# Performance work log

Hardware: AMD Instinct MI355X
Metric: run time of the kernel (lower is better)

Reference implementation:

```python
import jax, jax.numpy as jnp
import numpy as np

N = 100000      # nodes
E = 1600000     # edges (before self-loops)
IN = 128        # in_channels
HID = 64        # hidden_channels
HEADS = 2
G = 64          # graphs in batch
NEG_SLOPE = 0.2


def setup_inputs() -> dict:
    key = jax.random.key(0)
    ks = jax.random.split(key, 13)
    x = jax.random.normal(ks[0], (N, IN), dtype=jnp.float32)
    edge_index = jax.random.randint(ks[1], (2, E), 0, N, dtype=jnp.int64)
    batch = jnp.sort(jax.random.randint(ks[2], (N,), 0, G, dtype=jnp.int64))
    # GATConv 1: in=128 -> 64 per head, heads=2, concat
    W1 = jax.random.normal(ks[3], (IN, HEADS * HID), dtype=jnp.float32) / np.sqrt(IN)
    a1_src = jax.random.normal(ks[4], (HEADS, HID), dtype=jnp.float32) / np.sqrt(HID)
    a1_dst = jax.random.normal(ks[5], (HEADS, HID), dtype=jnp.float32) / np.sqrt(HID)
    b1 = jnp.zeros((HEADS * HID,), dtype=jnp.float32)
    # GATConv 2: in=128 -> 64, heads=1, mean (concat=False)
    W2 = jax.random.normal(ks[6], (HEADS * HID, 1 * HID), dtype=jnp.float32) / np.sqrt(HEADS * HID)
    a2_src = jax.random.normal(ks[7], (1, HID), dtype=jnp.float32) / np.sqrt(HID)
    a2_dst = jax.random.normal(ks[8], (1, HID), dtype=jnp.float32) / np.sqrt(HID)
    b2 = jnp.zeros((HID,), dtype=jnp.float32)
    # final Linear(64, 1)
    Wlin = jax.random.normal(ks[9], (HID, 1), dtype=jnp.float32) / np.sqrt(HID)
    blin = jnp.zeros((1,), dtype=jnp.float32)
    return {"x": x, "edge_index": edge_index, "batch": batch,
            "W1": W1, "a1_src": a1_src, "a1_dst": a1_dst, "b1": b1,
            "W2": W2, "a2_src": a2_src, "a2_dst": a2_dst, "b2": b2,
            "Wlin": Wlin, "blin": blin}


def gat_conv(x, src, dst, W, a_src, a_dst, bias, heads, out_dim, concat):
    # x: [N, F_in]; src/dst: [E'] (self-loops already included, PyG default)
    h = (x @ W).reshape(-1, heads, out_dim)                 # [N, H, C]
    alpha_s = jnp.sum(h * a_src[None], axis=-1)             # [N, H]
    alpha_d = jnp.sum(h * a_dst[None], axis=-1)             # [N, H]
    e = alpha_s[src] + alpha_d[dst]                         # [E', H]
    e = jnp.where(e > 0, e, NEG_SLOPE * e)                  # LeakyReLU(0.2)
    # segment softmax over incoming edges of each destination node
    e_max = jax.ops.segment_max(e, dst, num_segments=N)     # [N, H]
    e_exp = jnp.exp(e - e_max[dst])
    denom = jax.ops.segment_sum(e_exp, dst, num_segments=N) # [N, H]
    alpha = e_exp / denom[dst]                              # [E', H]
    msg = h[src] * alpha[..., None]                         # [E', H, C]
    out = jax.ops.segment_sum(msg, dst, num_segments=N)     # [N, H, C]
    if concat:
        out = out.reshape(-1, heads * out_dim)
    else:
        out = out.mean(axis=1)
    return out + bias


def reference(x, edge_index, batch, W1, a1_src, a1_dst, b1, W2, a2_src, a2_dst, b2, Wlin, blin):
    loops = jnp.arange(N, dtype=edge_index.dtype)
    src = jnp.concatenate([edge_index[0], loops])
    dst = jnp.concatenate([edge_index[1], loops])
    h = gat_conv(x, src, dst, W1, a1_src, a1_dst, b1, HEADS, HID, concat=True)
    h = jax.nn.relu(h)
    h = gat_conv(h, src, dst, W2, a2_src, a2_dst, b2, 1, HID, concat=False)
    h = jax.nn.relu(h)
    # global mean pool over graph ids
    sums = jax.ops.segment_sum(h, batch, num_segments=G)    # [G, HID]
    cnts = jax.ops.segment_sum(jnp.ones((N,), h.dtype), batch, num_segments=G)
    pooled = sums / jnp.maximum(cnts, 1.0)[:, None]
    return pooled @ Wlin + blin                             # [G, 1]
```

## Files before the change

kernel.cpp:

```cpp
#include <hip/hip_runtime.h>
#include <hip/hip_fp16.h>

#define NEG_SLOPE 0.2f
#define BSH 9
#define NBUCK 256
#define NB1 256
#define DCAP 12288

typedef _Float16 f16;
typedef __attribute__((ext_vector_type(8))) _Float16 half8;
typedef __attribute__((ext_vector_type(4))) _Float16 half4;
typedef __attribute__((ext_vector_type(4))) float f32x4;

__global__ __launch_bounds__(128) void prep_w(
    const float* __restrict__ W1, const float* __restrict__ W2,
    f16* __restrict__ W1t, f16* __restrict__ W2t)
{
    int b = blockIdx.x, k = threadIdx.x;
    if (b < 128) W1t[b * 128 + k] = (f16)W1[k * 128 + b];
    else { int c = b - 128; W2t[c * 128 + k] = (f16)W2[k * 64 + c]; }
}

__global__ __launch_bounds__(256) void gemm1_kernel(
    const float* __restrict__ x, const f16* __restrict__ W1t,
    const float* __restrict__ a1s_vec, const float* __restrict__ a1d_vec,
    f16* __restrict__ h1h, float* __restrict__ a1s, float* __restrict__ a1d, int N)
{
    __shared__ f16 Ash[64 * 136];
    __shared__ f16 Bsh[128 * 136];
    int t = threadIdx.x;
    int row0 = blockIdx.x << 6;

    #pragma unroll
    for (int c = 0; c < 8; ++c) {
        int l = c * 256 + t;
        int r = l >> 5, f = l & 31;
        int rr = row0 + r;
        float4 v = {0.f, 0.f, 0.f, 0.f};
        if (rr < N) v = *(const float4*)&x[(size_t)rr * 128 + f * 4];
        half4 hv = {(f16)v.x, (f16)v.y, (f16)v.z, (f16)v.w};
        *(half4*)&Ash[r * 136 + f * 4] = hv;
    }
    #pragma unroll
    for (int c = 0; c < 8; ++c) {
        int l = c * 256 + t;
        int row = l >> 4, f = l & 15;
        *(half8*)&Bsh[row * 136 + f * 8] = *(const half8*)&W1t[row * 128 + f * 8];
    }
    __syncthreads();

    int lane = t & 63, w = t >> 6;
    int lr = lane & 15, kg = lane >> 4;
    f32x4 acc[8];
    #pragma unroll
    for (int ct = 0; ct < 8; ++ct) acc[ct] = (f32x4){0.f, 0.f, 0.f, 0.f};

    #pragma unroll
    for (int kt = 0; kt < 4; ++kt) {
        half8 af = *(const half8*)&Ash[(w * 16 + lr) * 136 + kt * 32 + kg * 8];
        #pragma unroll
        for (int ct = 0; ct < 8; ++ct) {
            half8 bf = *(const half8*)&Bsh[(ct * 16 + lr) * 136 + kt * 32 + kg * 8];
            acc[ct] = __builtin_amdgcn_mfma_f32_16x16x32_f16(af, bf, acc[ct], 0, 0, 0);
        }
    }

    #pragma unroll
    for (int reg = 0; reg < 4; ++reg) {
        float ps0 = 0.f, pd0 = 0.f, ps1 = 0.f, pd1 = 0.f;
        #pragma unroll
        for (int ct = 0; ct < 4; ++ct) {
            float a = acc[ct][reg];
            ps0 += a * a1s_vec[ct * 16 + lr];
            pd0 += a * a1d_vec[ct * 16 + lr];
        }
        #pragma unroll
        for (int ct = 4; ct < 8; ++ct) {
            float a = acc[ct][reg];
            ps1 += a * a1s_vec[ct * 16 + lr];
            pd1 += a * a1d_vec[ct * 16 + lr];
        }
        #pragma unroll
        for (int o = 1; o <= 8; o <<= 1) {
            ps0 += __shfl_xor(ps0, o); pd0 += __shfl_xor(pd0, o);
            ps1 += __shfl_xor(ps1, o); pd1 += __shfl_xor(pd1, o);
        }
        if (lr == 0) {
            int rr = row0 + w * 16 + kg * 4 + reg;
            if (rr < N) {
                a1s[rr * 2] = ps0; a1d[rr * 2] = pd0;
                a1s[rr * 2 + 1] = ps1; a1d[rr * 2 + 1] = pd1;
            }
        }
    }

    __syncthreads();
    #pragma unroll
    for (int ct = 0; ct < 8; ++ct)
        #pragma unroll
        for (int reg = 0; reg < 4; ++reg)
            Ash[(w * 16 + kg * 4 + reg) * 136 + ct * 16 + lr] = (f16)acc[ct][reg];
    __syncthreads();
    #pragma unroll
    for (int c = 0; c < 4; ++c) {
        int l = c * 256 + t;
        int r = l >> 4, f = l & 15;
        int rr = row0 + r;
        if (rr < N) *(half8*)&h1h[(size_t)rr * 128 + f * 8] = *(const half8*)&Ash[r * 136 + f * 8];
    }
}

__global__ __launch_bounds__(256) void bucket_count(
    const int* __restrict__ ei, int* __restrict__ cntg, int E, int Ep, int chunk)
{
    __shared__ int lc[NBUCK];
    int i = blockIdx.x, t = threadIdx.x;
    lc[t] = 0;
    __syncthreads();
    int e0 = i * chunk, e1 = min(e0 + chunk, Ep);
    for (int e = e0 + t; e < e1; e += 256) {
        int dst = (e < E) ? ei[E + e] : e - E;
        atomicAdd(&lc[dst >> BSH], 1);
    }
    __syncthreads();
    cntg[i * NBUCK + t] = lc[t];
}

__global__ __launch_bounds__(256) void bucket_scan_t(
    const int* __restrict__ cntg, int* __restrict__ offs, int* __restrict__ tot)
{
    __shared__ int sh[256];
    int b = blockIdx.x, i = threadIdx.x;
    int v = cntg[i * NBUCK + b];
    sh[i] = v;
    __syncthreads();
    for (int off = 1; off < 256; off <<= 1) {
        int u = (i >= off) ? sh[i - off] : 0;
        __syncthreads();
        sh[i] += u;
        __syncthreads();
    }
    offs[i * NBUCK + b] = sh[i] - v;
    if (i == 255) tot[b] = sh[255];
}

__global__ __launch_bounds__(256) void bucket_base(
    const int* __restrict__ tot, int* __restrict__ bucketBase)
{
    __shared__ int sh[256];
    int b = threadIdx.x;
    int v = tot[b];
    sh[b] = v;
    __syncthreads();
    for (int off = 1; off < 256; off <<= 1) {
        int u = (b >= off) ? sh[b - off] : 0;
        __syncthreads();
        sh[b] += u;
        __syncthreads();
    }
    bucketBase[b] = sh[b] - v;
    if (b == 255) bucketBase[256] = sh[255];
}

__global__ __launch_bounds__(256) void bucket_place(
    const int* __restrict__ ei, const int* __restrict__ offs, const int* __restrict__ bucketBase,
    unsigned* __restrict__ pairs, int E, int Ep, int chunk)
{
    __shared__ int cur[NBUCK];
    int i = blockIdx.x, t = threadIdx.x;
    cur[t] = offs[i * NBUCK + t] + bucketBase[t];
    __syncthreads();
    int e0 = i * chunk, e1 = min(e0 + chunk, Ep);
    for (int e = e0 + t; e < e1; e += 256) {
        int src, dst;
        if (e < E) { src = ei[e]; dst = ei[E + e]; } else { src = dst = e - E; }
        int pos = atomicAdd(&cur[dst >> BSH], 1);
        pairs[pos] = ((unsigned)(dst & 511) << 17) | (unsigned)src;
    }
}

__global__ __launch_bounds__(256) void bucket_build(
    const unsigned* __restrict__ pairs, const int* __restrict__ bucketBase,
    int* __restrict__ rowStart, int* __restrict__ deg, int* __restrict__ srcS, int N)
{
    __shared__ int ucnt[512], ustart[512], sh[256];
    __shared__ unsigned stage[DCAP];
    int b = blockIdx.x, t = threadIdx.x;
    int node0 = b << BSH;
    if (node0 >= N) return;
    int s0 = bucketBase[b], s1 = bucketBase[b + 1];
    int cnt = s1 - s0;
    ucnt[t] = 0; ucnt[t + 256] = 0;
    __syncthreads();
    bool fit = (cnt <= DCAP);
    for (int k = t; k < cnt; k += 256) {
        unsigned v = pairs[s0 + k];
        if (fit) stage[k] = v;
        atomicAdd(&ucnt[v >> 17], 1);
    }
    __syncthreads();
    int a0 = ucnt[2 * t], a1 = ucnt[2 * t + 1];
    int s2 = a0 + a1;
    sh[t] = s2;
    __syncthreads();
    for (int off = 1; off < 256; off <<= 1) {
        int u = (t >= off) ? sh[t - off] : 0;
        __syncthreads();
        sh[t] += u;
        __syncthreads();
    }
    int exc = sh[t] - s2;
    ustart[2 * t] = exc;
    ustart[2 * t + 1] = exc + a0;
    __syncthreads();
    for (int l = t; l < 512; l += 256) {
        int node = node0 + l;
        if (node < N) { rowStart[node] = s0 + ustart[l]; deg[node] = ucnt[l]; }
    }
    __syncthreads();
    for (int k = t; k < cnt; k += 256) {
        unsigned v = fit ? stage[k] : pairs[s0 + k];
        int pos = atomicAdd(&ustart[v >> 17], 1);
        srcS[s0 + pos] = (int)(v & 131071u);
    }
}

__global__ __launch_bounds__(256) void fused_aggr1(
    const int* __restrict__ rowStart, const int* __restrict__ deg, const int* __restrict__ srcS,
    const float* __restrict__ a1s, const float* __restrict__ a1d,
    const f16* __restrict__ h1h, float* __restrict__ out1, int N)
{
    int lane = threadIdx.x & 63;
    int dst = blockIdx.x * 4 + (threadIdx.x >> 6);
    if (dst >= N) return;
    int base = rowStart[dst];
    int d = deg[dst];
    float ad0 = a1d[2 * dst], ad1 = a1d[2 * dst + 1];
    int tx = lane & 15, j2 = lane >> 4;
    float acc[8] = {};
    float dpart0 = 0.f, dpart1 = 0.f;

    for (int c0 = 0; c0 < d; c0 += 64) {
        int cn = min(64, d - c0);
        int s = 0; float p0 = 0.f, p1 = 0.f;
        if (lane < cn) {
            s = srcS[base + c0 + lane];
            float2 av = *(const float2*)&a1s[2 * s];
            float e0 = av.x + ad0, e1 = av.y + ad1;
            e0 = e0 > 0.f ? e0 : NEG_SLOPE * e0;
            e1 = e1 > 0.f ? e1 : NEG_SLOPE * e1;
            p0 = __expf(e0); p1 = __expf(e1);
        }
        dpart0 += p0; dpart1 += p1;
        int niter = (cn + 3) >> 2;
        #pragma unroll 4
        for (int jj = 0; jj < niter; ++jj) {
            int esub = jj * 4 + j2;
            int   sj = __shfl(s, esub);
            float q0 = __shfl(p0, esub);
            float q1 = __shfl(p1, esub);
            float q  = (tx < 8) ? q0 : q1;
            half8 v = *(const half8*)&h1h[(size_t)sj * 128 + tx * 8];
            #pragma unroll
            for (int k = 0; k < 8; ++k) acc[k] += q * (float)v[k];
        }
    }
    #pragma unroll
    for (int k = 0; k < 8; ++k) acc[k] += __shfl_xor(acc[k], 16);
    #pragma unroll
    for (int k = 0; k < 8; ++k) acc[k] += __shfl_xor(acc[k], 32);
    #pragma unroll
    for (int o = 32; o; o >>= 1) { dpart0 += __shfl_xor(dpart0, o); dpart1 += __shfl_xor(dpart1, o); }
    if (j2 == 0) {
        float iv = (tx < 8) ? (1.f / dpart0) : (1.f / dpart1);
        float4 lo = {acc[0] * iv, acc[1] * iv, acc[2] * iv, acc[3] * iv};
        float4 hi = {acc[4] * iv, acc[5] * iv, acc[6] * iv, acc[7] * iv};
        *(float4*)&out1[(size_t)dst * 128 + tx * 8] = lo;
        *(float4*)&out1[(size_t)dst * 128 + tx * 8 + 4] = hi;
    }
}

__global__ __launch_bounds__(256) void gemm2_kernel(
    const float* __restrict__ out1, const float* __restrict__ b1,
    const f16* __restrict__ W2t,
    const float* __restrict__ a2s_vec, const float* __restrict__ a2d_vec,
    f16* __restrict__ h2h, float* __restrict__ a2s, float* __restrict__ a2d, int N)
{
    __shared__ f16 Ash[64 * 136];
    __shared__ f16 Bsh[64 * 136];
    int t = threadIdx.x;
    int row0 = blockIdx.x << 6;

    #pragma unroll
    for (int c = 0; c < 8; ++c) {
        int l = c * 256 + t;
        int r = l >> 5, f = l & 31;
        int rr = row0 + r;
        float4 v = {0.f, 0.f, 0.f, 0.f};
        if (rr < N) {
            v = *(const float4*)&out1[(size_t)rr * 128 + f * 4];
            float4 bv = *(const float4*)&b1[f * 4];
            v.x = fmaxf(v.x + bv.x, 0.f);
            v.y = fmaxf(v.y + bv.y, 0.f);
            v.z = fmaxf(v.z + bv.z, 0.f);
            v.w = fmaxf(v.w + bv.w, 0.f);
        }
        half4 hv = {(f16)v.x, (f16)v.y, (f16)v.z, (f16)v.w};
        *(half4*)&Ash[r * 136 + f * 4] = hv;
    }
    #pragma unroll
    for (int c = 0; c < 4; ++c) {
        int l = c * 256 + t;
        int row = l >> 4, f = l & 15;
        *(half8*)&Bsh[row * 136 + f * 8] = *(const half8*)&W2t[row * 128 + f * 8];
    }
    __syncthreads();

    int lane = t & 63, w = t >> 6;
    int lr = lane & 15, kg = lane >> 4;
    f32x4 acc[4];
    #pragma unroll
    for (int ct = 0; ct < 4; ++ct) acc[ct] = (f32x4){0.f, 0.f, 0.f, 0.f};

    #pragma unroll
    for (int kt = 0; kt < 4; ++kt) {
        half8 af = *(const half8*)&Ash[(w * 16 + lr) * 136 + kt * 32 + kg * 8];
        #pragma unroll
        for (int ct = 0; ct < 4; ++ct) {
            half8 bf = *(const half8*)&Bsh[(ct * 16 + lr) * 136 + kt * 32 + kg * 8];
            acc[ct] = __builtin_amdgcn_mfma_f32_16x16x32_f16(af, bf, acc[ct], 0, 0, 0);
        }
    }

    #pragma unroll
    for (int reg = 0; reg < 4; ++reg) {
        float ps = 0.f, pd = 0.f;
        #pragma unroll
        for (int ct = 0; ct < 4; ++ct) {
            float a = acc[ct][reg];
            ps += a * a2s_vec[ct * 16 + lr];
            pd += a * a2d_vec[ct * 16 + lr];
        }
        #pragma unroll
        for (int o = 1; o <= 8; o <<= 1) { ps += __shfl_xor(ps, o); pd += __shfl_xor(pd, o); }
        if (lr == 0) {
            int rr = row0 + w * 16 + kg * 4 + reg;
            if (rr < N) { a2s[rr] = ps; a2d[rr] = pd; }
        }
    }

    __syncthreads();
    #pragma unroll
    for (int ct = 0; ct < 4; ++ct)
        #pragma unroll
        for (int reg = 0; reg < 4; ++reg)
            Ash[(w * 16 + kg * 4 + reg) * 136 + ct * 16 + lr] = (f16)acc[ct][reg];
    __syncthreads();
    #pragma unroll
    for (int c = 0; c < 2; ++c) {
        int l = c * 256 + t;
        int r = l >> 3, f = l & 7;
        int rr = row0 + r;
        if (rr < N) *(half8*)&h2h[(size_t)rr * 64 + f * 8] = *(const half8*)&Ash[r * 136 + f * 8];
    }
}

__global__ __launch_bounds__(256) void fused_aggr2(
    const int* __restrict__ rowStart, const int* __restrict__ deg, const int* __restrict__ srcS,
    const float* __restrict__ a2s, const float* __restrict__ a2d,
    const f16* __restrict__ h2h, float* __restrict__ out2, int N)
{
    int lane = threadIdx.x & 63;
    int dst = blockIdx.x * 4 + (threadIdx.x >> 6);
    if (dst >= N) return;
    int base = rowStart[dst];
    int d = deg[dst];
    float ad = a2d[dst];
    int tx = lane & 7, j3 = lane >> 3;
    float acc[8] = {};
    float dpart = 0.f;

    for (int c0 = 0; c0 < d; c0 += 64) {
        int cn = min(64, d - c0);
        int s = 0; float p = 0.f;
        if (lane < cn) {
            s = srcS[base + c0 + lane];
            float e = a2s[s] + ad;
            e = e > 0.f ? e : NEG_SLOPE * e;
            p = __expf(e);
        }
        dpart += p;
        int niter = (cn + 7) >> 3;
        #pragma unroll 4
        for (int jj = 0; jj < niter; ++jj) {
            int esub = jj * 8 + j3;
            int   sj = __shfl(s, esub);
            float q  = __shfl(p, esub);
            half8 v = *(const half8*)&h2h[(size_t)sj * 64 + tx * 8];
            #pragma unroll
            for (int k = 0; k < 8; ++k) acc[k] += q * (float)v[k];
        }
    }
    #pragma unroll
    for (int k = 0; k < 8; ++k) acc[k] += __shfl_xor(acc[k], 8);
    #pragma unroll
    for (int k = 0; k < 8; ++k) acc[k] += __shfl_xor(acc[k], 16);
    #pragma unroll
    for (int k = 0; k < 8; ++k) acc[k] += __shfl_xor(acc[k], 32);
    #pragma unroll
    for (int o = 32; o; o >>= 1) dpart += __shfl_xor(dpart, o);
    if (j3 == 0) {
        float iv = 1.f / dpart;
        float4 lo = {acc[0] * iv, acc[1] * iv, acc[2] * iv, acc[3] * iv};
        float4 hi = {acc[4] * iv, acc[5] * iv, acc[6] * iv, acc[7] * iv};
        *(float4*)&out2[(size_t)dst * 64 + tx * 8] = lo;
        *(float4*)&out2[(size_t)dst * 64 + tx * 8 + 4] = hi;
    }
}

__global__ __launch_bounds__(256) void pool_kernel(
    const float* __restrict__ out2, const float* __restrict__ b2,
    const int* __restrict__ batch, float* __restrict__ pool, float* __restrict__ cnt, int N)
{
    int lane = threadIdx.x & 63;
    int gwave = blockIdx.x * 4 + (threadIdx.x >> 6);
    int nwaves = gridDim.x * 4;
    int per = (N + nwaves - 1) / nwaves;
    int n0 = gwave * per;
    int n1 = min(n0 + per, N);
    if (n0 >= n1) return;
    float bb = b2[lane];
    float acc = 0.f;
    int count = 0;
    int gcur = batch[n0];
    for (int n = n0; n < n1; ++n) {
        int g = batch[n];
        if (g != gcur) {
            atomicAdd(&pool[gcur * 64 + lane], acc);
            if (lane == 0) atomicAdd(&cnt[gcur], (float)count);
            acc = 0.f; count = 0; gcur = g;
        }
        float v = out2[(size_t)n * 64 + lane] + bb;
        acc += v > 0.f ? v : 0.f;
        ++count;
    }
    atomicAdd(&pool[gcur * 64 + lane], acc);
    if (lane == 0) atomicAdd(&cnt[gcur], (float)count);
}

__global__ void final_kernel(
    const float* __restrict__ pool, const float* __restrict__ cnt,
    const float* __restrict__ Wlin, const float* __restrict__ blin,
    float* __restrict__ out, int G)
{
    int g = threadIdx.x;
    if (g >= G) return;
    float s = 0.f;
    #pragma unroll 8
    for (int c = 0; c < 64; ++c) s += pool[g * 64 + c] * Wlin[c];
    float cn = cnt[g]; cn = cn > 1.f ? cn : 1.f;
    out[g] = s / cn + blin[0];
}

extern "C" void kernel_launch(void* const* d_in, const int* in_sizes, int n_in,
                              void* d_out, int out_size, void* d_ws, size_t ws_size,
                              hipStream_t stream) {
    const float* x     = (const float*)d_in[0];
    const int*   ei    = (const int*)d_in[1];
    const int*   batch = (const int*)d_in[2];
    const float* W1    = (const float*)d_in[3];
    const float* a1sv  = (const float*)d_in[4];
    const float* a1dv  = (const float*)d_in[5];
    const float* b1    = (const float*)d_in[6];
    const float* W2    = (const float*)d_in[7];
    const float* a2sv  = (const float*)d_in[8];
    const float* a2dv  = (const float*)d_in[9];
    const float* b2    = (const float*)d_in[10];
    const float* Wlin  = (const float*)d_in[11];
    const float* blin  = (const float*)d_in[12];

    int N  = in_sizes[2];
    int E  = in_sizes[1] / 2;
    int Ep = E + N;
    const int G = 64;
    int chunk = (Ep + NB1 - 1) / NB1;

    float* ws = (float*)d_ws;
    size_t off = 0;
    float* out1 = ws + off; off += (size_t)N * 128;
    f16*  h1h   = (f16*)(ws + off); off += (size_t)N * 64;
    f16*  h2h   = (f16*)(ws + off); off += (size_t)N * 32;
    float* a1s  = ws + off; off += (size_t)N * 2;
    float* a1d  = ws + off; off += (size_t)N * 2;
    float* a2s  = ws + off; off += N;
    float* a2d  = ws + off; off += N;
    int* degA   = (int*)(ws + off); off += N;
    int* rowStart = (int*)(ws + off); off += N;
    int* cntg   = (int*)(ws + off); off += NB1 * NBUCK;
    int* offs   = (int*)(ws + off); off += NB1 * NBUCK;
    int* tot    = (int*)(ws + off); off += NBUCK;
    int* bucketBase = (int*)(ws + off); off += 257;
    unsigned* pairs = (unsigned*)(ws + off); off += Ep;
    int* srcS   = (int*)(ws + off); off += Ep;
    float* pool = ws + off; off += G * 64;
    float* cnt  = ws + off; off += G;
    f16* W1t    = (f16*)(ws + off); off += 128 * 64;
    f16* W2t    = (f16*)(ws + off); off += 64 * 64;
    float* out2 = (float*)h1h;

    hipMemsetAsync(pool, 0, (size_t)(G * 64 + G) * sizeof(float), stream);

    prep_w<<<192, 128, 0, stream>>>(W1, W2, W1t, W2t);

    bucket_count<<<NB1, 256, 0, stream>>>(ei, cntg, E, Ep, chunk);
    bucket_scan_t<<<NBUCK, 256, 0, stream>>>(cntg, offs, tot);
    bucket_base<<<1, 256, 0, stream>>>(tot, bucketBase);
    bucket_place<<<NB1, 256, 0, stream>>>(ei, offs, bucketBase, pairs, E, Ep, chunk);
    bucket_build<<<NBUCK, 256, 0, stream>>>(pairs, bucketBase, rowStart, degA, srcS, N);

    gemm1_kernel<<<(N + 63) / 64, 256, 0, stream>>>(x, W1t, a1sv, a1dv, h1h, a1s, a1d, N);
    fused_aggr1<<<(N + 3) / 4, 256, 0, stream>>>(rowStart, degA, srcS, a1s, a1d, h1h, out1, N);
    gemm2_kernel<<<(N + 63) / 64, 256, 0, stream>>>(out1, b1, W2t, a2sv, a2dv, h2h, a2s, a2d, N);
    fused_aggr2<<<(N + 3) / 4, 256, 0, stream>>>(rowStart, degA, srcS, a2s, a2d, h2h, out2, N);
    pool_kernel<<<256, 256, 0, stream>>>(out2, b2, batch, pool, cnt, N);
    final_kernel<<<1, 64, 0, stream>>>(pool, cnt, Wlin, blin, (float*)d_out, G);
}
```

Before: 274.9 us.

## Fuse bias+ReLU into aggregation epilogues, store fp16 intermediates, drop extra launches

Moves the bias add and ReLU of both GAT layers into the aggregation kernels' epilogues and writes the layer outputs as fp16 instead of fp32. That halves the intermediate traffic read by gemm2 and the pooling kernel. It also folds the bucket-base scan into bucket_place and bucket_build, and zeroes the pool buffer inside bucket_count, removing one kernel launch and one memset. The cost is extra fp16 rounding of the post-activation features and a redundant 256-element scan in every place and build block.

```diff
diff --git a/kernel.cpp b/kernel.cpp
--- a/kernel.cpp
+++ b/kernel.cpp
@@ -111,10 +111,12 @@
 }
 
 __global__ __launch_bounds__(256) void bucket_count(
-    const int* __restrict__ ei, int* __restrict__ cntg, int E, int Ep, int chunk)
+    const int* __restrict__ ei, int* __restrict__ cntg,
+    float* __restrict__ poolz, int nz, int E, int Ep, int chunk)
 {
     __shared__ int lc[NBUCK];
     int i = blockIdx.x, t = threadIdx.x;
+    if (i == 0) for (int z = t; z < nz; z += 256) poolz[z] = 0.f;
     lc[t] = 0;
     __syncthreads();
     int e0 = i * chunk, e1 = min(e0 + chunk, Ep);
@@ -144,31 +146,23 @@
     if (i == 255) tot[b] = sh[255];
 }
 
-__global__ __launch_bounds__(256) void bucket_base(
-    const int* __restrict__ tot, int* __restrict__ bucketBase)
-{
+__global__ __launch_bounds__(256) void bucket_place(
+    const int* __restrict__ ei, const int* __restrict__ offs, const int* __restrict__ tot,
+    unsigned* __restrict__ pairs, int E, int Ep, int chunk)
+{
+    __shared__ int cur[NBUCK];
     __shared__ int sh[256];
-    int b = threadIdx.x;
-    int v = tot[b];
-    sh[b] = v;
+    int i = blockIdx.x, t = threadIdx.x;
+    int v = tot[t];
+    sh[t] = v;
     __syncthreads();
     for (int off = 1; off < 256; off <<= 1) {
-        int u = (b >= off) ? sh[b - off] : 0;
-        __syncthreads();
-        sh[b] += u;
-        __syncthreads();
-    }
-    bucketBase[b] = sh[b] - v;
-    if (b == 255) bucketBase[256] = sh[255];
-}
-
-__global__ __launch_bounds__(256) void bucket_place(
-    const int* __restrict__ ei, const int* __restrict__ offs, const int* __restrict__ bucketBase,
-    unsigned* __restrict__ pairs, int E, int Ep, int chunk)
-{
-    __shared__ int cur[NBUCK];
-    int i = blockIdx.x, t = threadIdx.x;
-    cur[t] = offs[i * NBUCK + t] + bucketBase[t];
+        int u = (t >= off) ? sh[t - off] : 0;
+        __syncthreads();
+        sh[t] += u;
+        __syncthreads();
+    }
+    cur[t] = offs[i * NBUCK + t] + sh[t] - v;
     __syncthreads();
     int e0 = i * chunk, e1 = min(e0 + chunk, Ep);
     for (int e = e0 + t; e < e1; e += 256) {
@@ -180,7 +174,7 @@
 }
 
 __global__ __launch_bounds__(256) void bucket_build(
-    const unsigned* __restrict__ pairs, const int* __restrict__ bucketBase,
+    const unsigned* __restrict__ pairs, const int* __restrict__ tot,
     int* __restrict__ rowStart, int* __restrict__ deg, int* __restrict__ srcS, int N)
 {
     __shared__ int ucnt[512], ustart[512], sh[256];
@@ -188,15 +182,25 @@
     int b = blockIdx.x, t = threadIdx.x;
     int node0 = b << BSH;
     if (node0 >= N) return;
-    int s0 = bucketBase[b], s1 = bucketBase[b + 1];
+    ucnt[t] = 0; ucnt[t + 256] = 0;
+    int v = tot[t];
+    sh[t] = v;
+    __syncthreads();
+    for (int off = 1; off < 256; off <<= 1) {
+        int u = (t >= off) ? sh[t - off] : 0;
+        __syncthreads();
+        sh[t] += u;
+        __syncthreads();
+    }
+    int s0 = (b == 0) ? 0 : sh[b - 1];
+    int s1 = sh[b];
     int cnt = s1 - s0;
-    ucnt[t] = 0; ucnt[t + 256] = 0;
     __syncthreads();
     bool fit = (cnt <= DCAP);
     for (int k = t; k < cnt; k += 256) {
-        unsigned v = pairs[s0 + k];
-        if (fit) stage[k] = v;
-        atomicAdd(&ucnt[v >> 17], 1);
+        unsigned pv = pairs[s0 + k];
+        if (fit) stage[k] = pv;
+        atomicAdd(&ucnt[pv >> 17], 1);
     }
     __syncthreads();
     int a0 = ucnt[2 * t], a1 = ucnt[2 * t + 1];
@@ -219,16 +223,16 @@
     }
     __syncthreads();
     for (int k = t; k < cnt; k += 256) {
-        unsigned v = fit ? stage[k] : pairs[s0 + k];
-        int pos = atomicAdd(&ustart[v >> 17], 1);
-        srcS[s0 + pos] = (int)(v & 131071u);
+        unsigned pv = fit ? stage[k] : pairs[s0 + k];
+        int pos = atomicAdd(&ustart[pv >> 17], 1);
+        srcS[s0 + pos] = (int)(pv & 131071u);
     }
 }
 
 __global__ __launch_bounds__(256) void fused_aggr1(
     const int* __restrict__ rowStart, const int* __restrict__ deg, const int* __restrict__ srcS,
-    const float* __restrict__ a1s, const float* __restrict__ a1d,
-    const f16* __restrict__ h1h, float* __restrict__ out1, int N)
+    const float* __restrict__ a1s, const float* __restrict__ a1d, const float* __restrict__ b1,
+    const f16* __restrict__ h1h, f16* __restrict__ out1h, int N)
 {
     int lane = threadIdx.x & 63;
     int dst = blockIdx.x * 4 + (threadIdx.x >> 6);
@@ -273,16 +277,23 @@
     for (int o = 32; o; o >>= 1) { dpart0 += __shfl_xor(dpart0, o); dpart1 += __shfl_xor(dpart1, o); }
     if (j2 == 0) {
         float iv = (tx < 8) ? (1.f / dpart0) : (1.f / dpart1);
-        float4 lo = {acc[0] * iv, acc[1] * iv, acc[2] * iv, acc[3] * iv};
-        float4 hi = {acc[4] * iv, acc[5] * iv, acc[6] * iv, acc[7] * iv};
-        *(float4*)&out1[(size_t)dst * 128 + tx * 8] = lo;
-        *(float4*)&out1[(size_t)dst * 128 + tx * 8 + 4] = hi;
+        float4 blo = *(const float4*)&b1[tx * 8];
+        float4 bhi = *(const float4*)&b1[tx * 8 + 4];
+        float o0 = fmaxf(acc[0] * iv + blo.x, 0.f);
+        float o1 = fmaxf(acc[1] * iv + blo.y, 0.f);
+        float o2 = fmaxf(acc[2] * iv + blo.z, 0.f);
+        float o3 = fmaxf(acc[3] * iv + blo.w, 0.f);
+        float o4 = fmaxf(acc[4] * iv + bhi.x, 0.f);
+        float o5 = fmaxf(acc[5] * iv + bhi.y, 0.f);
+        float o6 = fmaxf(acc[6] * iv + bhi.z, 0.f);
+        float o7 = fmaxf(acc[7] * iv + bhi.w, 0.f);
+        half8 hv = {(f16)o0, (f16)o1, (f16)o2, (f16)o3, (f16)o4, (f16)o5, (f16)o6, (f16)o7};
+        *(half8*)&out1h[(size_t)dst * 128 + tx * 8] = hv;
     }
 }
 
 __global__ __launch_bounds__(256) void gemm2_kernel(
-    const float* __restrict__ out1, const float* __restrict__ b1,
-    const f16* __restrict__ W2t,
+    const f16* __restrict__ out1h, const f16* __restrict__ W2t,
     const float* __restrict__ a2s_vec, const float* __restrict__ a2d_vec,
     f16* __restrict__ h2h, float* __restrict__ a2s, float* __restrict__ a2d, int N)
 {
@@ -292,21 +303,13 @@
     int row0 = blockIdx.x << 6;
 
     #pragma unroll
-    for (int c = 0; c < 8; ++c) {
+    for (int c = 0; c < 4; ++c) {
         int l = c * 256 + t;
-        int r = l >> 5, f = l & 31;
+        int r = l >> 4, f = l & 15;
         int rr = row0 + r;
-        float4 v = {0.f, 0.f, 0.f, 0.f};
-        if (rr < N) {
-            v = *(const float4*)&out1[(size_t)rr * 128 + f * 4];
-            float4 bv = *(const float4*)&b1[f * 4];
-            v.x = fmaxf(v.x + bv.x, 0.f);
-            v.y = fmaxf(v.y + bv.y, 0.f);
-            v.z = fmaxf(v.z + bv.z, 0.f);
-            v.w = fmaxf(v.w + bv.w, 0.f);
-        }
-        half4 hv = {(f16)v.x, (f16)v.y, (f16)v.z, (f16)v.w};
-        *(half4*)&Ash[r * 136 + f * 4] = hv;
+        half8 hv = {0, 0, 0, 0, 0, 0, 0, 0};
+        if (rr < N) hv = *(const half8*)&out1h[(size_t)rr * 128 + f * 8];
+        *(half8*)&Ash[r * 136 + f * 8] = hv;
     }
     #pragma unroll
     for (int c = 0; c < 4; ++c) {
@@ -367,8 +370,8 @@
 
 __global__ __launch_bounds__(256) void fused_aggr2(
     const int* __restrict__ rowStart, const int* __restrict__ deg, const int* __restrict__ srcS,
-    const float* __restrict__ a2s, const float* __restrict__ a2d,
-    const f16* __restrict__ h2h, float* __restrict__ out2, int N)
+    const float* __restrict__ a2s, const float* __restrict__ a2d, const float* __restrict__ b2,
+    const f16* __restrict__ h2h, f16* __restrict__ out2h, int N)
 {
     int lane = threadIdx.x & 63;
     int dst = blockIdx.x * 4 + (threadIdx.x >> 6);
@@ -411,16 +414,24 @@
     for (int o = 32; o; o >>= 1) dpart += __shfl_xor(dpart, o);
     if (j3 == 0) {
         float iv = 1.f / dpart;
-        float4 lo = {acc[0] * iv, acc[1] * iv, acc[2] * iv, acc[3] * iv};
-        float4 hi = {acc[4] * iv, acc[5] * iv, acc[6] * iv, acc[7] * iv};
-        *(float4*)&out2[(size_t)dst * 64 + tx * 8] = lo;
-        *(float4*)&out2[(size_t)dst * 64 + tx * 8 + 4] = hi;
+        float4 blo = *(const float4*)&b2[tx * 8];
+        float4 bhi = *(const float4*)&b2[tx * 8 + 4];
+        float o0 = fmaxf(acc[0] * iv + blo.x, 0.f);
+        float o1 = fmaxf(acc[1] * iv + blo.y, 0.f);
+        float o2 = fmaxf(acc[2] * iv + blo.z, 0.f);
+        float o3 = fmaxf(acc[3] * iv + blo.w, 0.f);
+        float o4 = fmaxf(acc[4] * iv + bhi.x, 0.f);
+        float o5 = fmaxf(acc[5] * iv + bhi.y, 0.f);
+        float o6 = fmaxf(acc[6] * iv + bhi.z, 0.f);
+        float o7 = fmaxf(acc[7] * iv + bhi.w, 0.f);
+        half8 hv = {(f16)o0, (f16)o1, (f16)o2, (f16)o3, (f16)o4, (f16)o5, (f16)o6, (f16)o7};
+        *(half8*)&out2h[(size_t)dst * 64 + tx * 8] = hv;
     }
 }
 
 __global__ __launch_bounds__(256) void pool_kernel(
-    const float* __restrict__ out2, const float* __restrict__ b2,
-    const int* __restrict__ batch, float* __restrict__ pool, float* __restrict__ cnt, int N)
+    const f16* __restrict__ out2h, const int* __restrict__ batch,
+    float* __restrict__ pool, float* __restrict__ cnt, int N)
 {
     int lane = threadIdx.x & 63;
     int gwave = blockIdx.x * 4 + (threadIdx.x >> 6);
@@ -429,7 +440,6 @@
     int n0 = gwave * per;
     int n1 = min(n0 + per, N);
     if (n0 >= n1) return;
-    float bb = b2[lane];
     float acc = 0.f;
     int count = 0;
     int gcur = batch[n0];
@@ -440,8 +450,7 @@
             if (lane == 0) atomicAdd(&cnt[gcur], (float)count);
             acc = 0.f; count = 0; gcur = g;
         }
-        float v = out2[(size_t)n * 64 + lane] + bb;
-        acc += v > 0.f ? v : 0.f;
+        acc += (float)out2h[(size_t)n * 64 + lane];
         ++count;
     }
     atomicAdd(&pool[gcur * 64 + lane], acc);
@@ -487,7 +496,7 @@
 
     float* ws = (float*)d_ws;
     size_t off = 0;
-    float* out1 = ws + off; off += (size_t)N * 128;
+    f16*  out1h = (f16*)(ws + off); off += (size_t)N * 64;
     f16*  h1h   = (f16*)(ws + off); off += (size_t)N * 64;
     f16*  h2h   = (f16*)(ws + off); off += (size_t)N * 32;
     float* a1s  = ws + off; off += (size_t)N * 2;
@@ -499,29 +508,25 @@
     int* cntg   = (int*)(ws + off); off += NB1 * NBUCK;
     int* offs   = (int*)(ws + off); off += NB1 * NBUCK;
     int* tot    = (int*)(ws + off); off += NBUCK;
-    int* bucketBase = (int*)(ws + off); off += 257;
     unsigned* pairs = (unsigned*)(ws + off); off += Ep;
     int* srcS   = (int*)(ws + off); off += Ep;
     float* pool = ws + off; off += G * 64;
     float* cnt  = ws + off; off += G;
     f16* W1t    = (f16*)(ws + off); off += 128 * 64;
     f16* W2t    = (f16*)(ws + off); off += 64 * 64;
-    float* out2 = (float*)h1h;
-
-    hipMemsetAsync(pool, 0, (size_t)(G * 64 + G) * sizeof(float), stream);
+    f16* out2h  = h1h;
 
     prep_w<<<192, 128, 0, stream>>>(W1, W2, W1t, W2t);
 
-    bucket_count<<<NB1, 256, 0, stream>>>(ei, cntg, E, Ep, chunk);
+    bucket_count<<<NB1, 256, 0, stream>>>(ei, cntg, pool, G * 64 + G, E, Ep, chunk);
     bucket_scan_t<<<NBUCK, 256, 0, stream>>>(cntg, offs, tot);
-    bucket_base<<<1, 256, 0, stream>>>(tot, bucketBase);
-    bucket_place<<<NB1, 256, 0, stream>>>(ei, offs, bucketBase, pairs, E, Ep, chunk);
-    bucket_build<<<NBUCK, 256, 0, stream>>>(pairs, bucketBase, rowStart, degA, srcS, N);
+    bucket_place<<<NB1, 256, 0, stream>>>(ei, offs, tot, pairs, E, Ep, chunk);
+    bucket_build<<<NBUCK, 256, 0, stream>>>(pairs, tot, rowStart, degA, srcS, N);
 
     gemm1_kernel<<<(N + 63) / 64, 256, 0, stream>>>(x, W1t, a1sv, a1dv, h1h, a1s, a1d, N);
-    fused_aggr1<<<(N + 3) / 4, 256, 0, stream>>>(rowStart, degA, srcS, a1s, a1d, h1h, out1, N);
-    gemm2_kernel<<<(N + 63) / 64, 256, 0, stream>>>(out1, b1, W2t, a2sv, a2dv, h2h, a2s, a2d, N);
-    fused_aggr2<<<(N + 3) / 4, 256, 0, stream>>>(rowStart, degA, srcS, a2s, a2d, h2h, out2, N);
-    pool_kernel<<<256, 256, 0, stream>>>(out2, b2, batch, pool, cnt, N);
+    fused_aggr1<<<(N + 3) / 4, 256, 0, stream>>>(rowStart, degA, srcS, a1s, a1d, b1, h1h, out1h, N);
+    gemm2_kernel<<<(N + 63) / 64, 256, 0, stream>>>(out1h, W2t, a2sv, a2dv, h2h, a2s, a2d, N);
+    fused_aggr2<<<(N + 3) / 4, 256, 0, stream>>>(rowStart, degA, srcS, a2s, a2d, b2, h2h, out2h, N);
+    pool_kernel<<<256, 256, 0, stream>>>(out2h, batch, pool, cnt, N);
     final_kernel<<<1, 64, 0, stream>>>(pool, cnt, Wlin, blin, (float*)d_out, G);
 }
```

New measurement: 264.6 us. 3.7% less time.
